# Performance work log

Measured on AMD Instinct MI355X. Metric: run time of the kernel, lower is better.

## Reference

```python
import jax, jax.numpy as jnp
import numpy as np

_HIST_BINS = 64
TOP_K_FRAC = 0.125
HIST_THRESHOLD = 2048


def setup_inputs() -> dict:
    key = jax.random.key(0)
    B, S = 256, 131072
    importance = jax.random.normal(key, (B, S), dtype=jnp.float32)
    return {"importance": importance, "S": S}


def reference(importance, S):
    # importance: [B, S] float32; S: python int
    K = max(1, int(TOP_K_FRAC * S))
    if S > HIST_THRESHOLD:
        # Histogram bookkeeping path (computed but unused by the original module;
        # reproduced here for faithfulness to the source's memory traffic).
        imin = jnp.min(importance, axis=-1, keepdims=True)  # [B,1]
        imax = jnp.max(importance, axis=-1, keepdims=True)  # [B,1]
        rng = jnp.clip(imax - imin, 1e-8, None)
        bin_idx = ((importance - imin) / rng * (_HIST_BINS - 1)).astype(jnp.int32)
        bin_idx = jnp.clip(bin_idx, 0, _HIST_BINS - 1)  # [B,S]
        B = importance.shape[0]
        rows = jnp.arange(B)[:, None]  # [B,1] broadcast against [B,S]
        hist = jnp.zeros((B, _HIST_BINS), dtype=jnp.int32).at[rows, bin_idx].add(1)
        del hist  # dead value, exactly as in the torch source
    _, top_idx = jax.lax.top_k(importance, K)  # [B,K] indices into last dim
    return (top_idx, K)
```

## Files before the change

kernel.cpp:

```cpp
#include <hip/hip_runtime.h>
#include <stdint.h>


#define S_LEN   131072
#define K_SEL   16384
#define NBINS   8192
#define LOWBITS 19
#define IDXMASK 0x1FFFFu
#define CAND_CAP 20480
#define SORT_CAP 4096
#define DIRECT_MAX 256
#define WL_PER_ROW 2048
#define D_GRID  2048
#define HCAP 256
#define LCAP 512
#define NWAVE 16
#define PC_WAVE 1664
#define NITER (S_LEN / 4 / 1024)
#define U0_THRESH 0xBF880000u
#define BU0 (U0_THRESH >> LOWBITS)

__device__ __forceinline__ unsigned int ordered_u32(float f) {
  unsigned int x = __float_as_uint(f);
  unsigned int mask = (unsigned int)((int)x >> 31) | 0x80000000u;
  return x ^ mask;
}

__device__ __forceinline__ void suffix_scan_8k(const unsigned int* h,
                                               unsigned int* sfx,
                                               unsigned int* waveTot,
                                               unsigned int* sb1p,
                                               int tid, int lane, int wave) {
  if (tid == 0) *sb1p = 0xFFFFFFFFu;
  uint4 c0 = *(const uint4*)&h[tid * 8];
  uint4 c1 = *(const uint4*)&h[tid * 8 + 4];
  unsigned int v[8] = {c0.x, c0.y, c0.z, c0.w, c1.x, c1.y, c1.z, c1.w};
#pragma unroll
  for (int s = 6; s >= 0; --s) v[s] += v[s + 1];
  unsigned int tot = v[0];
  unsigned int suf = tot;
#pragma unroll
  for (int d = 1; d < 64; d <<= 1) {
    unsigned int o = __shfl_down(suf, d, 64);
    if (lane + d < 64) suf += o;
  }
  if (lane == 0) waveTot[wave] = suf;
  __syncthreads();
  unsigned int carry = 0;
  for (int w2 = wave + 1; w2 < NWAVE; ++w2) carry += waveTot[w2];
  unsigned int addv = (suf - tot) + carry;
  {
    uint4 o0 = make_uint4(v[0] + addv, v[1] + addv, v[2] + addv, v[3] + addv);
    uint4 o1 = make_uint4(v[4] + addv, v[5] + addv, v[6] + addv, v[7] + addv);
    *(uint4*)&sfx[tid * 8]     = o0;
    *(uint4*)&sfx[tid * 8 + 4] = o1;
  }
  __syncthreads();
#pragma unroll
  for (int s = 0; s < 8; ++s) {
    int b = tid * 8 + s;
    unsigned int cur = sfx[b];
    unsigned int nxt = (b + 1 < NBINS) ? sfx[b + 1] : 0u;
    if (cur >= K_SEL && nxt < K_SEL) *sb1p = (unsigned int)b;
  }
  __syncthreads();
}

__global__ __launch_bounds__(1024)
void select_kernel(const float* __restrict__ in,
                   unsigned long long* __restrict__ pairs,
                   unsigned long long* __restrict__ cand,
                   uint4* __restrict__ wl, unsigned int* __restrict__ ctrs,
                   unsigned int wlHalf, int* __restrict__ out,
                   int B, long long out_size) {
  const int row  = blockIdx.x;
  const int tid  = threadIdx.x;
  const int lane = tid & 63, wave = tid >> 6;
  __shared__ unsigned int h[NBINS];
  __shared__ unsigned int sfx[NBINS];
  __shared__ unsigned int waveTot[NWAVE];
  __shared__ unsigned int wcnt[NWAVE];
  __shared__ unsigned int sb1, nH, nL, gHs, gLs, sovf;
  __shared__ uint2 lheavy[HCAP];
  __shared__ uint2 llight[LCAP];

  for (int i = tid; i < NBINS; i += 1024) h[i] = 0;
  if (tid == 0) { nH = 0; nL = 0; sovf = 0; }
  __syncthreads();

  const float4* p = (const float4*)(in + (size_t)row * S_LEN);
  unsigned long long* seg = pairs + ((size_t)row * NWAVE + wave) * PC_WAVE;
  unsigned int base = 0;
  const unsigned long long lmask = (1ull << lane) - 1ull;

#define CAP1(U, IDX) do {                                                    \
    unsigned int u_ = (U);                                                   \
    bool pred_ = (u_ >= U0_THRESH);                                          \
    unsigned long long m_ = __ballot(pred_);                                 \
    if (pred_) {                                                             \
      unsigned int pos_ = base + (unsigned int)__popcll(m_ & lmask);         \
      if (pos_ < PC_WAVE)                                                    \
        seg[pos_] = ((unsigned long long)u_ << 17) |                         \
                    (unsigned long long)(IDXMASK - (unsigned int)(IDX));     \
    }                                                                        \
    base += (unsigned int)__popcll(m_); } while (0)

#define CAP4(V, I4) do { int idx0_ = (I4) * 4;                               \
    CAP1(ordered_u32((V).x), idx0_ + 0);                                     \
    CAP1(ordered_u32((V).y), idx0_ + 1);                                     \
    CAP1(ordered_u32((V).z), idx0_ + 2);                                     \
    CAP1(ordered_u32((V).w), idx0_ + 3); } while (0)

#pragma unroll 2
  for (int it = 0; it < NITER; it += 4) {
    int i0 = it * 1024 + tid;
    float4 L0 = p[i0];
    float4 L1 = p[i0 + 1024];
    float4 L2 = p[i0 + 2048];
    float4 L3 = p[i0 + 3072];
    CAP4(L0, i0);
    CAP4(L1, i0 + 1024);
    CAP4(L2, i0 + 2048);
    CAP4(L3, i0 + 3072);
  }
  if (lane == 0) {
    wcnt[wave] = base;
    if (base > PC_WAVE) sovf = 1u;
  }
  __syncthreads();
  const bool ovf = (sovf != 0u);

  if (!ovf) {
    const unsigned int myN = wcnt[wave];
    for (unsigned int i = (unsigned int)lane; i < myN; i += 64u)
      atomicAdd(&h[(unsigned int)(seg[i] >> 36)], 1u);
  } else {
    for (int it = 0; it < NITER; ++it) {
      float4 v4 = p[it * 1024 + tid];
      float f[4] = {v4.x, v4.y, v4.z, v4.w};
#pragma unroll
      for (int e = 0; e < 4; ++e)
        atomicAdd(&h[ordered_u32(f[e]) >> LOWBITS], 1u);
    }
  }
  __syncthreads();

  suffix_scan_8k(h, sfx, waveTot, &sb1, tid, lane, wave);
  bool found1 = (sb1 != 0xFFFFFFFFu);
  if (!found1) {
    for (int it = 0; it < NITER; ++it) {
      float4 v4 = p[it * 1024 + tid];
      float f[4] = {v4.x, v4.y, v4.z, v4.w};
#pragma unroll
      for (int e = 0; e < 4; ++e) {
        unsigned int u = ordered_u32(f[e]);
        if (u < U0_THRESH) atomicAdd(&h[u >> LOWBITS], 1u);
      }
    }
    __syncthreads();
    suffix_scan_8k(h, sfx, waveTot, &sb1, tid, lane, wave);
  }
  const unsigned int b1 = sb1;
  const bool fast = found1 && !ovf;

  for (int i = tid; i < NBINS; i += 1024) {
    unsigned int end   = sfx[i];
    unsigned int start = (i + 1 < NBINS) ? sfx[i + 1] : 0u;
    h[i] = start;
    if ((unsigned int)i >= b1) {
      unsigned int cnt2 = end - start;
      if (cnt2) {
        if (cnt2 > DIRECT_MAX) {
          unsigned int p2 = atomicAdd(&nH, 1u);
          if (p2 < HCAP) lheavy[p2] = make_uint2(start, end);
          else {
            unsigned int g = atomicAdd(&ctrs[0], 1u);
            if (g < wlHalf) wl[2 * wlHalf - 1 - g] = make_uint4((unsigned int)row, start, end, 0u);
          }
        } else {
          unsigned int p2 = atomicAdd(&nL, 1u);
          if (p2 < LCAP) llight[p2] = make_uint2(start, end);
          else {
            unsigned int g = atomicAdd(&ctrs[1], 1u);
            if (g < wlHalf) wl[g] = make_uint4((unsigned int)row, start, end, 0u);
          }
        }
      }
    }
  }
  __syncthreads();
  if (tid == 0) {
    gHs = atomicAdd(&ctrs[0], nH < HCAP ? nH : HCAP);
    gLs = atomicAdd(&ctrs[1], nL < LCAP ? nL : LCAP);
  }
  __syncthreads();
  {
    unsigned int hN = nH < HCAP ? nH : HCAP;
    unsigned int lN = nL < LCAP ? nL : LCAP;
    for (unsigned int i = tid; i < hN; i += 1024) {
      uint2 e = lheavy[i]; unsigned int pos = gHs + i;
      if (pos < wlHalf) wl[2 * wlHalf - 1 - pos] = make_uint4((unsigned int)row, e.x, e.y, 0u);
    }
    for (unsigned int i = tid; i < lN; i += 1024) {
      uint2 e = llight[i]; unsigned int pos = gLs + i;
      if (pos < wlHalf) wl[pos] = make_uint4((unsigned int)row, e.x, e.y, 0u);
    }
  }

  unsigned long long* c = cand + (size_t)row * CAND_CAP;
  if (fast) {
    const unsigned int myN = wcnt[wave];
    for (unsigned int i = (unsigned int)lane; i < myN; i += 64u) {
      unsigned long long k = seg[i];
      unsigned int b = (unsigned int)(k >> 36);
      if (b >= b1) {
        unsigned int pos = atomicAdd(&h[b], 1u);
        if (pos < CAND_CAP) c[pos] = k;
      }
    }
  } else {
    for (int it = 0; it < NITER; ++it) {
      int i4 = it * 1024 + tid;
      float4 v4 = p[i4];
      int idx0 = i4 * 4;
      float f[4] = {v4.x, v4.y, v4.z, v4.w};
#pragma unroll
      for (int e = 0; e < 4; ++e) {
        unsigned int u = ordered_u32(f[e]);
        unsigned int b = u >> LOWBITS;
        if (b >= b1) {
          unsigned int pos = atomicAdd(&h[b], 1u);
          unsigned long long key =
              ((unsigned long long)u << 17) |
              (unsigned long long)(IDXMASK - (unsigned int)(idx0 + e));
          if (pos < CAND_CAP) c[pos] = key;
        }
      }
    }
  }
  if (row == 0 && tid == 0) {
    long long pos = (long long)B * K_SEL;
    if (pos < out_size) out[pos] = K_SEL;
  }
#undef CAP1
#undef CAP4
}

__global__ __launch_bounds__(256)
void sort_kernel(const uint4* __restrict__ wl, const unsigned int* __restrict__ ctrs,
                 unsigned int wlHalf, const unsigned long long* __restrict__ cand,
                 int* __restrict__ out) {
  const int tid  = threadIdx.x;
  const int lane = tid & 63, wave = tid >> 6;
  __shared__ unsigned int   skey2[SORT_CAP];
  __shared__ unsigned char  sdig2[SORT_CAP];
  __shared__ unsigned int   ssfx[257];
  __shared__ unsigned int   scur[256];
  __shared__ unsigned int   segTot[4];
  unsigned int nHeavy = ctrs[0]; if (nHeavy > wlHalf) nHeavy = wlHalf;
  unsigned int nLight = ctrs[1]; if (nLight > wlHalf) nLight = wlHalf;

  for (unsigned int w = blockIdx.x; w < nHeavy; w += gridDim.x) {
    const uint4 it = wl[2 * wlHalf - 1 - w];
    const unsigned int row = it.x, start = it.y;
    unsigned int count = it.z - start;
    if (count > SORT_CAP) count = SORT_CAP;
    const unsigned long long* c = cand + (size_t)row * CAND_CAP + start;
    int* orow = out + (size_t)row * K_SEL;

    unsigned long long me[16];
#pragma unroll
    for (int j = 0; j < 16; ++j) {
      unsigned int i = (unsigned int)tid + 256u * j;
      me[j] = (i < count) ? c[i] : 0ull;
    }
    scur[tid] = 0;
    __syncthreads();
#pragma unroll
    for (int j = 0; j < 16; ++j) {
      unsigned int i = (unsigned int)tid + 256u * j;
      if (i < count) atomicAdd(&scur[(unsigned int)(me[j] >> 28) & 255u], 1u);
    }
    __syncthreads();
    unsigned int cnt = scur[tid];
    unsigned int suf = cnt;
#pragma unroll
    for (int d = 1; d < 64; d <<= 1) {
      unsigned int o = __shfl_down(suf, d, 64);
      if (lane + d < 64) suf += o;
    }
    if (lane == 0) segTot[wave] = suf;
    __syncthreads();
    unsigned int carry = 0;
    for (int w2 = wave + 1; w2 < 4; ++w2) carry += segTot[w2];
    ssfx[tid] = suf + carry;
    if (tid == 0) ssfx[256] = 0;
    __syncthreads();
    scur[tid] = ssfx[tid + 1];
    __syncthreads();
#pragma unroll
    for (int j = 0; j < 16; ++j) {
      unsigned int i = (unsigned int)tid + 256u * j;
      if (i < count) {
        unsigned long long k = me[j];
        unsigned int d = (unsigned int)(k >> 28) & 255u;
        unsigned int p = atomicAdd(&scur[d], 1u);
        skey2[p] = (unsigned int)k & 0x0FFFFFFFu;
        sdig2[p] = (unsigned char)d;
      }
    }
    __syncthreads();
    for (unsigned int p = tid; p < count; p += 256) {
      unsigned int k = skey2[p];
      unsigned int d = sdig2[p];
      unsigned int lo = ssfx[d + 1], hi = ssfx[d];
      unsigned int r = 0;
      for (unsigned int q = lo; q < hi; ++q) r += (skey2[q] > k) ? 1u : 0u;
      unsigned int pos = start + lo + r;
      if (pos < K_SEL)
        orow[pos] = (int)(IDXMASK - (k & IDXMASK));
    }
    __syncthreads();
  }

  for (unsigned int w = blockIdx.x * 4u + (unsigned int)wave; w < nLight;
       w += gridDim.x * 4u) {
    const uint4 it = wl[w];
    const unsigned int row = it.x, start = it.y;
    const unsigned int count = it.z - start;
    const unsigned long long* c = cand + (size_t)row * CAND_CAP + start;
    int* orow = out + (size_t)row * K_SEL;
    if (count <= 64) {
      unsigned long long me = ((unsigned int)lane < count) ? c[lane] : 0ull;
      unsigned int r = 0;
      for (int l = 0; l < 64; ++l)
        r += (__shfl(me, l, 64) > me) ? 1u : 0u;
      if ((unsigned int)lane < count) {
        unsigned int pos = start + r;
        if (pos < K_SEL)
          orow[pos] = (int)(IDXMASK - ((unsigned int)me & IDXMASK));
      }
    } else if (count <= 128) {
      unsigned long long me[2];
#pragma unroll
      for (int e = 0; e < 2; ++e) {
        unsigned int i = (unsigned int)lane + 64u * e;
        me[e] = (i < count) ? c[i] : 0ull;
      }
      unsigned int r[2] = {0u, 0u};
#pragma unroll
      for (int e = 0; e < 2; ++e) {
        for (int l = 0; l < 64; ++l) {
          unsigned long long kj = __shfl(me[e], l, 64);
#pragma unroll
          for (int e2 = 0; e2 < 2; ++e2) r[e2] += (kj > me[e2]) ? 1u : 0u;
        }
      }
#pragma unroll
      for (int e = 0; e < 2; ++e) {
        unsigned int i = (unsigned int)lane + 64u * e;
        if (i < count) {
          unsigned int pos = start + r[e];
          if (pos < K_SEL)
            orow[pos] = (int)(IDXMASK - ((unsigned int)me[e] & IDXMASK));
        }
      }
    } else {
      unsigned long long me[4];
#pragma unroll
      for (int e = 0; e < 4; ++e) {
        unsigned int i = (unsigned int)lane + 64u * e;
        me[e] = (i < count) ? c[i] : 0ull;
      }
      unsigned int r[4] = {0u, 0u, 0u, 0u};
#pragma unroll
      for (int e = 0; e < 4; ++e) {
        for (int l = 0; l < 64; ++l) {
          unsigned long long kj = __shfl(me[e], l, 64);
#pragma unroll
          for (int e2 = 0; e2 < 4; ++e2) r[e2] += (kj > me[e2]) ? 1u : 0u;
        }
      }
#pragma unroll
      for (int e = 0; e < 4; ++e) {
        unsigned int i = (unsigned int)lane + 64u * e;
        if (i < count) {
          unsigned int pos = start + r[e];
          if (pos < K_SEL)
            orow[pos] = (int)(IDXMASK - ((unsigned int)me[e] & IDXMASK));
        }
      }
    }
  }
}

extern "C" void kernel_launch(void* const* d_in, const int* in_sizes, int n_in,
                              void* d_out, int out_size, void* d_ws, size_t ws_size,
                              hipStream_t stream) {
  const float* importance = (const float*)d_in[0];
  int B = in_sizes[0] / S_LEN;
  if (B < 1) B = 1;
  (void)n_in; (void)ws_size;

  const unsigned int wlCap  = (unsigned int)B * WL_PER_ROW;
  const unsigned int wlHalf = wlCap / 2;
  size_t pairBytes = (size_t)B * NWAVE * PC_WAVE * sizeof(unsigned long long);
  size_t candBytes = (size_t)B * CAND_CAP * sizeof(unsigned long long);
  size_t wlBytes   = (size_t)wlCap * sizeof(uint4);
  char* base = (char*)d_ws;
  unsigned long long* pairs = (unsigned long long*)base;
  unsigned long long* cand  = (unsigned long long*)(base + pairBytes);
  uint4* wl                 = (uint4*)(base + pairBytes + candBytes);
  unsigned int* ctrs        = (unsigned int*)(base + pairBytes + candBytes + wlBytes);
  int* out = (int*)d_out;

  hipMemsetAsync(ctrs, 0, 4 * sizeof(unsigned int), stream);
  select_kernel<<<dim3(B),      dim3(1024), 0, stream>>>(
      importance, pairs, cand, wl, ctrs, wlHalf, out, B, (long long)out_size);
  sort_kernel  <<<dim3(D_GRID), dim3(256),  0, stream>>>(wl, ctrs, wlHalf, cand, out);
}
```

Baseline: 273.6 us.

## Split capture pass into multi-block-per-row kernel with fused histogram

The single per-row select kernel is split in two. A new capture kernel runs 8 blocks of 256 threads per row, compacting candidates above the fixed threshold and building a high-bin histogram in shared memory that is merged into a global per-row histogram with atomics. A second scan/gather kernel loads that histogram instead of re-reading the captured pairs to rebuild it. The intent is to get more parallelism and better bandwidth use than one 1024-thread block per row, at the cost of an extra launch, global atomics and a larger memset.

```diff
diff --git a/kernel.cpp b/kernel.cpp
--- a/kernel.cpp
+++ b/kernel.cpp
@@ -14,16 +14,75 @@
 #define D_GRID  2048
 #define HCAP 256
 #define LCAP 512
-#define NWAVE 16
-#define PC_WAVE 1664
-#define NITER (S_LEN / 4 / 1024)
 #define U0_THRESH 0xBF880000u
-#define BU0 (U0_THRESH >> LOWBITS)
+#define HI0  6128
+#define NHI  (NBINS - HI0)
+#define NCH     8
+#define CH_LEN  (S_LEN / NCH)
+#define K1ITER  (CH_LEN / 4 / 256)
+#define NSEG    (NCH * 4)
+#define PC_SEG  832
 
 __device__ __forceinline__ unsigned int ordered_u32(float f) {
   unsigned int x = __float_as_uint(f);
   unsigned int mask = (unsigned int)((int)x >> 31) | 0x80000000u;
   return x ^ mask;
+}
+
+__global__ __launch_bounds__(256)
+void capture_kernel(const float* __restrict__ in,
+                    unsigned long long* __restrict__ pairs,
+                    unsigned int* __restrict__ segcnt,
+                    unsigned int* __restrict__ rowhist,
+                    unsigned int* __restrict__ rowflag) {
+  const int row   = blockIdx.x >> 3;
+  const int chunk = blockIdx.x & 7;
+  const int tid   = threadIdx.x;
+  const int lane  = tid & 63, wave = tid >> 6;
+  __shared__ unsigned int hh[NHI];
+  for (int i = tid; i < NHI; i += 256) hh[i] = 0;
+  __syncthreads();
+
+  const float4* p = (const float4*)(in + (size_t)row * S_LEN + (size_t)chunk * CH_LEN);
+  unsigned long long* seg =
+      pairs + ((size_t)row * NSEG + (size_t)(chunk * 4 + wave)) * PC_SEG;
+  unsigned int base = 0;
+  const unsigned long long lmask = (1ull << lane) - 1ull;
+
+#define CAP1(U, IDX) do {                                                    \
+    unsigned int u_ = (U);                                                   \
+    bool pred_ = (u_ >= U0_THRESH);                                          \
+    unsigned long long m_ = __ballot(pred_);                                 \
+    if (pred_) {                                                             \
+      atomicAdd(&hh[(u_ >> LOWBITS) - HI0], 1u);                             \
+      unsigned int pos_ = base + (unsigned int)__popcll(m_ & lmask);         \
+      if (pos_ < PC_SEG)                                                     \
+        seg[pos_] = ((unsigned long long)u_ << 17) |                         \
+                    (unsigned long long)(IDXMASK - (unsigned int)(IDX));     \
+    }                                                                        \
+    base += (unsigned int)__popcll(m_); } while (0)
+
+#pragma unroll 2
+  for (int it = 0; it < K1ITER; ++it) {
+    int i4 = it * 256 + tid;
+    float4 v = p[i4];
+    int idx0 = chunk * CH_LEN + i4 * 4;
+    CAP1(ordered_u32(v.x), idx0 + 0);
+    CAP1(ordered_u32(v.y), idx0 + 1);
+    CAP1(ordered_u32(v.z), idx0 + 2);
+    CAP1(ordered_u32(v.w), idx0 + 3);
+  }
+#undef CAP1
+  if (lane == 0) {
+    segcnt[row * NSEG + chunk * 4 + wave] = base;
+    if (base > PC_SEG) rowflag[row] = 1u;
+  }
+  __syncthreads();
+  unsigned int* rh = rowhist + (size_t)row * NHI;
+  for (int i = tid; i < NHI; i += 256) {
+    unsigned int c = hh[i];
+    if (c) atomicAdd(&rh[i], c);
+  }
 }
 
 __device__ __forceinline__ void suffix_scan_8k(const unsigned int* h,
@@ -47,7 +106,7 @@
   if (lane == 0) waveTot[wave] = suf;
   __syncthreads();
   unsigned int carry = 0;
-  for (int w2 = wave + 1; w2 < NWAVE; ++w2) carry += waveTot[w2];
+  for (int w2 = wave + 1; w2 < 16; ++w2) carry += waveTot[w2];
   unsigned int addv = (suf - tot) + carry;
   {
     uint4 o0 = make_uint4(v[0] + addv, v[1] + addv, v[2] + addv, v[3] + addv);
@@ -67,88 +126,49 @@
 }
 
 __global__ __launch_bounds__(1024)
-void select_kernel(const float* __restrict__ in,
-                   unsigned long long* __restrict__ pairs,
-                   unsigned long long* __restrict__ cand,
-                   uint4* __restrict__ wl, unsigned int* __restrict__ ctrs,
-                   unsigned int wlHalf, int* __restrict__ out,
-                   int B, long long out_size) {
+void scan_gather_kernel(const float* __restrict__ in,
+                        const unsigned long long* __restrict__ pairs,
+                        const unsigned int* __restrict__ segcnt,
+                        const unsigned int* __restrict__ rowhist,
+                        const unsigned int* __restrict__ rowflag,
+                        unsigned long long* __restrict__ cand,
+                        uint4* __restrict__ wl, unsigned int* __restrict__ ctrs,
+                        unsigned int wlHalf, int* __restrict__ out,
+                        int B, long long out_size) {
   const int row  = blockIdx.x;
   const int tid  = threadIdx.x;
   const int lane = tid & 63, wave = tid >> 6;
   __shared__ unsigned int h[NBINS];
   __shared__ unsigned int sfx[NBINS];
-  __shared__ unsigned int waveTot[NWAVE];
-  __shared__ unsigned int wcnt[NWAVE];
-  __shared__ unsigned int sb1, nH, nL, gHs, gLs, sovf;
+  __shared__ unsigned int waveTot[16];
+  __shared__ unsigned int sb1, nH, nL, gHs, gLs;
   __shared__ uint2 lheavy[HCAP];
   __shared__ uint2 llight[LCAP];
 
-  for (int i = tid; i < NBINS; i += 1024) h[i] = 0;
-  if (tid == 0) { nH = 0; nL = 0; sovf = 0; }
-  __syncthreads();
-
+  for (int i = tid; i < HI0; i += 1024) h[i] = 0;
+  for (int i = tid; i < NHI; i += 1024) h[HI0 + i] = rowhist[(size_t)row * NHI + i];
+  if (tid == 0) { nH = 0; nL = 0; }
+  __syncthreads();
+
+  const bool ovf = (rowflag[row] != 0u);
   const float4* p = (const float4*)(in + (size_t)row * S_LEN);
-  unsigned long long* seg = pairs + ((size_t)row * NWAVE + wave) * PC_WAVE;
-  unsigned int base = 0;
-  const unsigned long long lmask = (1ull << lane) - 1ull;
-
-#define CAP1(U, IDX) do {                                                    \
-    unsigned int u_ = (U);                                                   \
-    bool pred_ = (u_ >= U0_THRESH);                                          \
-    unsigned long long m_ = __ballot(pred_);                                 \
-    if (pred_) {                                                             \
-      unsigned int pos_ = base + (unsigned int)__popcll(m_ & lmask);         \
-      if (pos_ < PC_WAVE)                                                    \
-        seg[pos_] = ((unsigned long long)u_ << 17) |                         \
-                    (unsigned long long)(IDXMASK - (unsigned int)(IDX));     \
-    }                                                                        \
-    base += (unsigned int)__popcll(m_); } while (0)
-
-#define CAP4(V, I4) do { int idx0_ = (I4) * 4;                               \
-    CAP1(ordered_u32((V).x), idx0_ + 0);                                     \
-    CAP1(ordered_u32((V).y), idx0_ + 1);                                     \
-    CAP1(ordered_u32((V).z), idx0_ + 2);                                     \
-    CAP1(ordered_u32((V).w), idx0_ + 3); } while (0)
-
-#pragma unroll 2
-  for (int it = 0; it < NITER; it += 4) {
-    int i0 = it * 1024 + tid;
-    float4 L0 = p[i0];
-    float4 L1 = p[i0 + 1024];
-    float4 L2 = p[i0 + 2048];
-    float4 L3 = p[i0 + 3072];
-    CAP4(L0, i0);
-    CAP4(L1, i0 + 1024);
-    CAP4(L2, i0 + 2048);
-    CAP4(L3, i0 + 3072);
-  }
-  if (lane == 0) {
-    wcnt[wave] = base;
-    if (base > PC_WAVE) sovf = 1u;
-  }
-  __syncthreads();
-  const bool ovf = (sovf != 0u);
-
-  if (!ovf) {
-    const unsigned int myN = wcnt[wave];
-    for (unsigned int i = (unsigned int)lane; i < myN; i += 64u)
-      atomicAdd(&h[(unsigned int)(seg[i] >> 36)], 1u);
-  } else {
-    for (int it = 0; it < NITER; ++it) {
+  if (ovf) {
+    for (int i = tid; i < NBINS; i += 1024) h[i] = 0;
+    __syncthreads();
+    for (int it = 0; it < 32; ++it) {
       float4 v4 = p[it * 1024 + tid];
       float f[4] = {v4.x, v4.y, v4.z, v4.w};
 #pragma unroll
       for (int e = 0; e < 4; ++e)
         atomicAdd(&h[ordered_u32(f[e]) >> LOWBITS], 1u);
     }
-  }
-  __syncthreads();
+    __syncthreads();
+  }
 
   suffix_scan_8k(h, sfx, waveTot, &sb1, tid, lane, wave);
   bool found1 = (sb1 != 0xFFFFFFFFu);
   if (!found1) {
-    for (int it = 0; it < NITER; ++it) {
+    for (int it = 0; it < 32; ++it) {
       float4 v4 = p[it * 1024 + tid];
       float f[4] = {v4.x, v4.y, v4.z, v4.w};
 #pragma unroll
@@ -209,17 +229,22 @@
 
   unsigned long long* c = cand + (size_t)row * CAND_CAP;
   if (fast) {
-    const unsigned int myN = wcnt[wave];
-    for (unsigned int i = (unsigned int)lane; i < myN; i += 64u) {
-      unsigned long long k = seg[i];
-      unsigned int b = (unsigned int)(k >> 36);
-      if (b >= b1) {
-        unsigned int pos = atomicAdd(&h[b], 1u);
-        if (pos < CAND_CAP) c[pos] = k;
+#pragma unroll
+    for (int sI = 0; sI < 2; ++sI) {
+      const int s = wave * 2 + sI;
+      const unsigned int cntS = segcnt[row * NSEG + s];
+      const unsigned long long* sg = pairs + ((size_t)row * NSEG + s) * PC_SEG;
+      for (unsigned int i = (unsigned int)lane; i < cntS; i += 64u) {
+        unsigned long long k = sg[i];
+        unsigned int b = (unsigned int)(k >> 36);
+        if (b >= b1) {
+          unsigned int pos = atomicAdd(&h[b], 1u);
+          if (pos < CAND_CAP) c[pos] = k;
+        }
       }
     }
   } else {
-    for (int it = 0; it < NITER; ++it) {
+    for (int it = 0; it < 32; ++it) {
       int i4 = it * 1024 + tid;
       float4 v4 = p[i4];
       int idx0 = i4 * 4;
@@ -242,8 +267,6 @@
     long long pos = (long long)B * K_SEL;
     if (pos < out_size) out[pos] = K_SEL;
   }
-#undef CAP1
-#undef CAP4
 }
 
 __global__ __launch_bounds__(256)
@@ -404,18 +427,27 @@
 
   const unsigned int wlCap  = (unsigned int)B * WL_PER_ROW;
   const unsigned int wlHalf = wlCap / 2;
-  size_t pairBytes = (size_t)B * NWAVE * PC_WAVE * sizeof(unsigned long long);
+  size_t pairBytes = (size_t)B * NSEG * PC_SEG * sizeof(unsigned long long);
   size_t candBytes = (size_t)B * CAND_CAP * sizeof(unsigned long long);
   size_t wlBytes   = (size_t)wlCap * sizeof(uint4);
+  size_t segcBytes = (size_t)B * NSEG * sizeof(unsigned int);
   char* base = (char*)d_ws;
   unsigned long long* pairs = (unsigned long long*)base;
   unsigned long long* cand  = (unsigned long long*)(base + pairBytes);
   uint4* wl                 = (uint4*)(base + pairBytes + candBytes);
-  unsigned int* ctrs        = (unsigned int*)(base + pairBytes + candBytes + wlBytes);
+  unsigned int* segcnt      = (unsigned int*)(base + pairBytes + candBytes + wlBytes);
+  unsigned int* ctrs        = segcnt + (size_t)B * NSEG;
+  unsigned int* rowflag     = ctrs + 4;
+  unsigned int* rowhist     = rowflag + B;
+  size_t zeroBytes = (4 + (size_t)B + (size_t)B * NHI) * sizeof(unsigned int);
   int* out = (int*)d_out;
-
-  hipMemsetAsync(ctrs, 0, 4 * sizeof(unsigned int), stream);
-  select_kernel<<<dim3(B),      dim3(1024), 0, stream>>>(
-      importance, pairs, cand, wl, ctrs, wlHalf, out, B, (long long)out_size);
-  sort_kernel  <<<dim3(D_GRID), dim3(256),  0, stream>>>(wl, ctrs, wlHalf, cand, out);
-}
+  (void)segcBytes;
+
+  hipMemsetAsync(ctrs, 0, zeroBytes, stream);
+  capture_kernel<<<dim3(B * NCH), dim3(256), 0, stream>>>(
+      importance, pairs, segcnt, rowhist, rowflag);
+  scan_gather_kernel<<<dim3(B), dim3(1024), 0, stream>>>(
+      importance, pairs, segcnt, rowhist, rowflag, cand, wl, ctrs, wlHalf,
+      out, B, (long long)out_size);
+  sort_kernel<<<dim3(D_GRID), dim3(256), 0, stream>>>(wl, ctrs, wlHalf, cand, out);
+}
```

Result: no change. 275.7 us (+0.8%).
